# Performance work log

Hardware: AMD Instinct MI355X
Metric: run time of the kernel (lower is better)

The kernel has to match this reference:

```python
import jax, jax.numpy as jnp
import numpy as np

TEMPERATURE = 0.1
EPS = 1e-12  # matches F.normalize eps clamp


def setup_inputs() -> dict:
    key = jax.random.key(0)
    k1, k2 = jax.random.split(key)
    B, D = 4096, 1024
    z1 = jax.random.normal(k1, (B, D), dtype=jnp.float32)
    z2 = jax.random.normal(k2, (B, D), dtype=jnp.float32)
    return {"z1": z1, "z2": z2}


def reference(z1, z2):
    B = z1.shape[0]
    # L2-normalize rows (F.normalize dim=1, eps clamp)
    n1 = z1 / jnp.maximum(jnp.linalg.norm(z1, axis=1, keepdims=True), EPS)
    n2 = z2 / jnp.maximum(jnp.linalg.norm(z2, axis=1, keepdims=True), EPS)
    reps = jnp.concatenate([n1, n2], axis=0)  # [2B, D]
    # Rows are unit-norm, so cosine similarity == dot product -> one GEMM
    sim = (reps @ reps.T) / TEMPERATURE  # [2B, 2B]
    # positives: diag offsets +B and -B
    pos = jnp.concatenate([jnp.diagonal(sim, B), jnp.diagonal(sim, -B)])  # [2B]
    # logits row i = [pos_i, sim[i, j != i]]. logsumexp over that set =
    # logaddexp(pos_i, logsumexp over the row with the main diagonal removed).
    eye = jnp.eye(2 * B, dtype=bool)
    masked = jnp.where(eye, -jnp.inf, sim)
    lse_neg = jax.scipy.special.logsumexp(masked, axis=1)  # [2B]
    lse = jnp.logaddexp(pos, lse_neg)
    # CrossEntropyLoss with labels==0 -> mean(lse - logit_0) = mean(lse - pos)
    return jnp.mean(lse - pos)
```

## Files before the change

### kernel.cpp

```cpp
#include <hip/hip_runtime.h>

#define D_DIM 1024
#define B_HALF 4096
#define NROWS 8192
#define INV_TEMP 10.0f

typedef __bf16 bf16x8 __attribute__((ext_vector_type(8)));
typedef float floatx4 __attribute__((ext_vector_type(4)));

__device__ __forceinline__ unsigned short f32_to_bf16(float f) {
    union { float f; unsigned u; } v; v.f = f;
    unsigned r = 0x7FFFu + ((v.u >> 16) & 1u);
    return (unsigned short)((v.u + r) >> 16);
}

__global__ __launch_bounds__(256) void normalize_kernel(
    const float* __restrict__ z1, const float* __restrict__ z2,
    unsigned short* __restrict__ R)
{
    const int row = blockIdx.x;
    const int tid = threadIdx.x;
    const float* src = (row < B_HALF) ? (z1 + (size_t)row * D_DIM)
                                      : (z2 + (size_t)(row - B_HALF) * D_DIM);
    float4 v = ((const float4*)src)[tid];
    float ss = v.x * v.x + v.y * v.y + v.z * v.z + v.w * v.w;
    #pragma unroll
    for (int off = 32; off > 0; off >>= 1) ss += __shfl_down(ss, off);
    __shared__ float wsum[4];
    if ((tid & 63) == 0) wsum[tid >> 6] = ss;
    __syncthreads();
    float tot = wsum[0] + wsum[1] + wsum[2] + wsum[3];
    float scale = 1.0f / fmaxf(sqrtf(tot), 1e-12f);
    ushort4 o;
    o.x = f32_to_bf16(v.x * scale);
    o.y = f32_to_bf16(v.y * scale);
    o.z = f32_to_bf16(v.z * scale);
    o.w = f32_to_bf16(v.w * scale);
    ((ushort4*)(R + (size_t)row * D_DIM))[tid] = o;
}

__global__ __launch_bounds__(256) void gemm_lse_kernel(
    const unsigned short* __restrict__ R,
    float* __restrict__ partial, float* __restrict__ pos)
{
    __shared__ unsigned short As[128 * 32];
    __shared__ unsigned short Bs[128 * 32];
    __shared__ float rowsum[2][128];
    __shared__ float colsum[2][128];

    const int t = blockIdx.x;
    int rt = (int)((129.0f - sqrtf((float)(16641 - 8 * t))) * 0.5f);
    while ((rt + 1) * 64 - (rt + 1) * rt / 2 <= t) ++rt;
    while (rt * 64 - rt * (rt - 1) / 2 > t) --rt;
    const int ct = rt + (t - (rt * 64 - rt * (rt - 1) / 2));
    const bool isDiag = (rt == ct);

    const int tid = threadIdx.x;
    const int wave = tid >> 6, lane = tid & 63;
    const int wm = wave >> 1, wn = wave & 1;
    const int row0 = rt * 128, col0 = ct * 128;

    floatx4 acc[4][4] = {};

    const int lrow = lane >> 2;
    const int lk = (lane & 3) * 8;
    const unsigned short* gA = R + (size_t)row0 * D_DIM;
    const unsigned short* gB = R + (size_t)col0 * D_DIM;

    const int lm = lane & 15;
    const int lq = lane >> 4;

    for (int k0 = 0; k0 < D_DIM; k0 += 32) {
        #pragma unroll
        for (int rnd = 0; rnd < 2; ++rnd) {
            const int c = rnd * 4 + wave;
            const int grow = c * 16 + lrow;
            __builtin_amdgcn_global_load_lds(
                (const __attribute__((address_space(1))) unsigned int*)(gA + (size_t)grow * D_DIM + k0 + lk),
                (__attribute__((address_space(3))) unsigned int*)(As + c * 512),
                16, 0, 0);
            __builtin_amdgcn_global_load_lds(
                (const __attribute__((address_space(1))) unsigned int*)(gB + (size_t)grow * D_DIM + k0 + lk),
                (__attribute__((address_space(3))) unsigned int*)(Bs + c * 512),
                16, 0, 0);
        }
        __syncthreads();

        bf16x8 af[4], bfr[4];
        #pragma unroll
        for (int i = 0; i < 4; ++i) {
            af[i]  = *(const bf16x8*)(As + (wm * 64 + i * 16 + lm) * 32 + lq * 8);
            bfr[i] = *(const bf16x8*)(Bs + (wn * 64 + i * 16 + lm) * 32 + lq * 8);
        }
        #pragma unroll
        for (int mi = 0; mi < 4; ++mi)
            #pragma unroll
            for (int ni = 0; ni < 4; ++ni)
                acc[mi][ni] = __builtin_amdgcn_mfma_f32_16x16x32_bf16(
                    af[mi], bfr[ni], acc[mi][ni], 0, 0, 0);
        __syncthreads();
    }

    float ecol[4] = {0.0f, 0.0f, 0.0f, 0.0f};
    #pragma unroll
    for (int mi = 0; mi < 4; ++mi) {
        #pragma unroll
        for (int reg = 0; reg < 4; ++reg) {
            const int gr = row0 + wm * 64 + mi * 16 + lq * 4 + reg;
            float esum = 0.0f;
            #pragma unroll
            for (int ni = 0; ni < 4; ++ni) {
                const int gc = col0 + wn * 64 + ni * 16 + lm;
                float s = acc[mi][ni][reg] * INV_TEMP;
                if (gc == gr + B_HALF) { pos[gr] = s; pos[gc] = s; }
                float e = (gc == gr) ? 0.0f : __expf(s);
                esum += e;
                ecol[ni] += e;
            }
            esum += __shfl_xor(esum, 1);
            esum += __shfl_xor(esum, 2);
            esum += __shfl_xor(esum, 4);
            esum += __shfl_xor(esum, 8);
            if (lm == 0) rowsum[wn][wm * 64 + mi * 16 + lq * 4 + reg] = esum;
        }
    }
    #pragma unroll
    for (int ni = 0; ni < 4; ++ni) {
        ecol[ni] += __shfl_xor(ecol[ni], 16);
        ecol[ni] += __shfl_xor(ecol[ni], 32);
    }
    if (lq == 0 && !isDiag) {
        #pragma unroll
        for (int ni = 0; ni < 4; ++ni)
            colsum[wm][wn * 64 + ni * 16 + lm] = ecol[ni];
    }
    __syncthreads();
    if (tid < 128) {
        partial[(size_t)(row0 + tid) * 64 + ct] = rowsum[0][tid] + rowsum[1][tid];
        if (!isDiag)
            partial[(size_t)(col0 + tid) * 64 + rt] = colsum[0][tid] + colsum[1][tid];
    }
}

__global__ __launch_bounds__(256) void finalize_kernel(
    const float* __restrict__ partial, const float* __restrict__ pos,
    float* __restrict__ out)
{
    const int r = blockIdx.x * 256 + threadIdx.x;
    const float4* p = (const float4*)(partial + (size_t)r * 64);
    float S = 0.0f;
    #pragma unroll
    for (int i = 0; i < 16; ++i) { float4 v = p[i]; S += (v.x + v.y) + (v.z + v.w); }
    const float po = pos[r];
    float contrib = log1pf(S * __expf(-po));
    #pragma unroll
    for (int off = 32; off > 0; off >>= 1) contrib += __shfl_down(contrib, off);
    __shared__ float wsum[4];
    if ((threadIdx.x & 63) == 0) wsum[threadIdx.x >> 6] = contrib;
    __syncthreads();
    if (threadIdx.x == 0)
        atomicAdd(out, (wsum[0] + wsum[1] + wsum[2] + wsum[3]) * (1.0f / 8192.0f));
}

extern "C" void kernel_launch(void* const* d_in, const int* in_sizes, int n_in,
                              void* d_out, int out_size, void* d_ws, size_t ws_size,
                              hipStream_t stream)
{
    const float* z1 = (const float*)d_in[0];
    const float* z2 = (const float*)d_in[1];
    float* out = (float*)d_out;
    char* ws = (char*)d_ws;
    unsigned short* R = (unsigned short*)ws;
    float* partial = (float*)(ws + (size_t)16 * 1024 * 1024);
    float* pos     = (float*)(ws + (size_t)18 * 1024 * 1024);

    hipMemsetAsync(d_out, 0, sizeof(float), stream);
    normalize_kernel<<<NROWS, 256, 0, stream>>>(z1, z2, R);
    gemm_lse_kernel<<<2080, 256, 0, stream>>>(R, partial, pos);
    finalize_kernel<<<32, 256, 0, stream>>>(partial, pos, out);
}
```

Before: 174.7 us.

## Fuse normalize, GEMM-LSE and finalize into one persistent cooperative kernel

Replaces the three-kernel pipeline with a single cooperative persistent kernel. It normalizes rows, synchronizes the grid, hands out triangular GEMM tiles through an atomic work counter, synchronizes again, and finalizes the loss in block 0. Per-tile row and column exp-sums now go to a per-row float array via atomics, replacing the 64-wide partial buffer. This is meant to remove launch overhead, the memset and the partial-sum traffic. In exchange it adds grid-sync cost, atomic contention, a serial single-block finalize, and nondeterministic float summation order. A fallback three-kernel path runs only if the cooperative launch fails.

```diff
diff --git a/kernel.cpp b/kernel.cpp
--- a/kernel.cpp
+++ b/kernel.cpp
@@ -1,9 +1,13 @@
 #include <hip/hip_runtime.h>
+#include <hip/hip_cooperative_groups.h>
+
+namespace cg = cooperative_groups;
 
 #define D_DIM 1024
 #define B_HALF 4096
 #define NROWS 8192
 #define INV_TEMP 10.0f
+#define NTILES 2080
 
 typedef __bf16 bf16x8 __attribute__((ext_vector_type(8)));
 typedef float floatx4 __attribute__((ext_vector_type(4)));
@@ -14,61 +18,33 @@
     return (unsigned short)((v.u + r) >> 16);
 }
 
-__global__ __launch_bounds__(256) void normalize_kernel(
-    const float* __restrict__ z1, const float* __restrict__ z2,
-    unsigned short* __restrict__ R)
-{
-    const int row = blockIdx.x;
-    const int tid = threadIdx.x;
-    const float* src = (row < B_HALF) ? (z1 + (size_t)row * D_DIM)
-                                      : (z2 + (size_t)(row - B_HALF) * D_DIM);
-    float4 v = ((const float4*)src)[tid];
-    float ss = v.x * v.x + v.y * v.y + v.z * v.z + v.w * v.w;
-    #pragma unroll
-    for (int off = 32; off > 0; off >>= 1) ss += __shfl_down(ss, off);
-    __shared__ float wsum[4];
-    if ((tid & 63) == 0) wsum[tid >> 6] = ss;
-    __syncthreads();
-    float tot = wsum[0] + wsum[1] + wsum[2] + wsum[3];
-    float scale = 1.0f / fmaxf(sqrtf(tot), 1e-12f);
-    ushort4 o;
-    o.x = f32_to_bf16(v.x * scale);
-    o.y = f32_to_bf16(v.y * scale);
-    o.z = f32_to_bf16(v.z * scale);
-    o.w = f32_to_bf16(v.w * scale);
-    ((ushort4*)(R + (size_t)row * D_DIM))[tid] = o;
-}
-
-__global__ __launch_bounds__(256) void gemm_lse_kernel(
-    const unsigned short* __restrict__ R,
-    float* __restrict__ partial, float* __restrict__ pos)
+__device__ __forceinline__ void process_tile(
+    int t, const unsigned short* __restrict__ R,
+    float* __restrict__ Srow, float* __restrict__ pos, int tid)
 {
     __shared__ unsigned short As[128 * 32];
     __shared__ unsigned short Bs[128 * 32];
     __shared__ float rowsum[2][128];
     __shared__ float colsum[2][128];
 
-    const int t = blockIdx.x;
+    const int wave = tid >> 6, lane = tid & 63;
+    const int wm = wave >> 1, wn = wave & 1;
+    const int lrow = lane >> 2;
+    const int lk = (lane & 3) * 8;
+    const int lm = lane & 15;
+    const int lq = lane >> 4;
+
     int rt = (int)((129.0f - sqrtf((float)(16641 - 8 * t))) * 0.5f);
     while ((rt + 1) * 64 - (rt + 1) * rt / 2 <= t) ++rt;
     while (rt * 64 - rt * (rt - 1) / 2 > t) --rt;
     const int ct = rt + (t - (rt * 64 - rt * (rt - 1) / 2));
     const bool isDiag = (rt == ct);
-
-    const int tid = threadIdx.x;
-    const int wave = tid >> 6, lane = tid & 63;
-    const int wm = wave >> 1, wn = wave & 1;
     const int row0 = rt * 128, col0 = ct * 128;
 
-    floatx4 acc[4][4] = {};
-
-    const int lrow = lane >> 2;
-    const int lk = (lane & 3) * 8;
     const unsigned short* gA = R + (size_t)row0 * D_DIM;
     const unsigned short* gB = R + (size_t)col0 * D_DIM;
 
-    const int lm = lane & 15;
-    const int lq = lane >> 4;
+    floatx4 acc[4][4] = {};
 
     for (int k0 = 0; k0 < D_DIM; k0 += 32) {
         #pragma unroll
@@ -136,27 +112,117 @@
     }
     __syncthreads();
     if (tid < 128) {
-        partial[(size_t)(row0 + tid) * 64 + ct] = rowsum[0][tid] + rowsum[1][tid];
+        unsafeAtomicAdd(&Srow[row0 + tid], rowsum[0][tid] + rowsum[1][tid]);
         if (!isDiag)
-            partial[(size_t)(col0 + tid) * 64 + rt] = colsum[0][tid] + colsum[1][tid];
-    }
+            unsafeAtomicAdd(&Srow[col0 + tid], colsum[0][tid] + colsum[1][tid]);
+    }
+    __syncthreads();
+}
+
+__global__ __launch_bounds__(256) void fused_kernel(
+    const float* __restrict__ z1, const float* __restrict__ z2,
+    unsigned short* __restrict__ R, float* __restrict__ Srow,
+    float* __restrict__ pos, unsigned int* __restrict__ ctr,
+    float* __restrict__ out)
+{
+    __shared__ float red[4];
+    __shared__ int s_t;
+    const int tid = threadIdx.x;
+    const int bid = blockIdx.x;
+    const int nb = gridDim.x;
+    const int wave = tid >> 6, lane = tid & 63;
+
+    if (bid == 0 && tid == 0) ctr[0] = 0u;
+    for (int row = bid; row < NROWS; row += nb) {
+        const float* src = (row < B_HALF) ? (z1 + (size_t)row * D_DIM)
+                                          : (z2 + (size_t)(row - B_HALF) * D_DIM);
+        float4 v = ((const float4*)src)[tid];
+        float ss = v.x * v.x + v.y * v.y + v.z * v.z + v.w * v.w;
+        #pragma unroll
+        for (int off = 32; off > 0; off >>= 1) ss += __shfl_down(ss, off);
+        if (lane == 0) red[wave] = ss;
+        __syncthreads();
+        float tot = red[0] + red[1] + red[2] + red[3];
+        float scale = 1.0f / fmaxf(sqrtf(tot), 1e-12f);
+        ushort4 o;
+        o.x = f32_to_bf16(v.x * scale);
+        o.y = f32_to_bf16(v.y * scale);
+        o.z = f32_to_bf16(v.z * scale);
+        o.w = f32_to_bf16(v.w * scale);
+        ((ushort4*)(R + (size_t)row * D_DIM))[tid] = o;
+        if (tid == 0) Srow[row] = 0.0f;
+        __syncthreads();
+    }
+    cg::this_grid().sync();
+
+    for (;;) {
+        if (tid == 0) s_t = (int)atomicAdd(ctr, 1u);
+        __syncthreads();
+        const int t = s_t;
+        if (t >= NTILES) break;
+        process_tile(t, R, Srow, pos, tid);
+    }
+    cg::this_grid().sync();
+
+    if (bid == 0) {
+        float c = 0.0f;
+        for (int r = tid; r < NROWS; r += 256)
+            c += log1pf(Srow[r] * __expf(-pos[r]));
+        #pragma unroll
+        for (int off = 32; off > 0; off >>= 1) c += __shfl_down(c, off);
+        __syncthreads();
+        if (lane == 0) red[wave] = c;
+        __syncthreads();
+        if (tid == 0)
+            out[0] = (red[0] + red[1] + red[2] + red[3]) * (1.0f / 8192.0f);
+    }
+}
+
+__global__ __launch_bounds__(256) void normalize_kernel(
+    const float* __restrict__ z1, const float* __restrict__ z2,
+    unsigned short* __restrict__ R, float* __restrict__ Srow,
+    float* __restrict__ out)
+{
+    const int row = blockIdx.x;
+    const int tid = threadIdx.x;
+    if (row == 0 && tid == 0) out[0] = 0.0f;
+    const float* src = (row < B_HALF) ? (z1 + (size_t)row * D_DIM)
+                                      : (z2 + (size_t)(row - B_HALF) * D_DIM);
+    float4 v = ((const float4*)src)[tid];
+    float ss = v.x * v.x + v.y * v.y + v.z * v.z + v.w * v.w;
+    #pragma unroll
+    for (int off = 32; off > 0; off >>= 1) ss += __shfl_down(ss, off);
+    __shared__ float wsum[4];
+    if ((tid & 63) == 0) wsum[tid >> 6] = ss;
+    __syncthreads();
+    float tot = wsum[0] + wsum[1] + wsum[2] + wsum[3];
+    float scale = 1.0f / fmaxf(sqrtf(tot), 1e-12f);
+    ushort4 o;
+    o.x = f32_to_bf16(v.x * scale);
+    o.y = f32_to_bf16(v.y * scale);
+    o.z = f32_to_bf16(v.z * scale);
+    o.w = f32_to_bf16(v.w * scale);
+    ((ushort4*)(R + (size_t)row * D_DIM))[tid] = o;
+    if (tid == 0) Srow[row] = 0.0f;
+}
+
+__global__ __launch_bounds__(256) void gemm_kernel(
+    const unsigned short* __restrict__ R,
+    float* __restrict__ Srow, float* __restrict__ pos)
+{
+    process_tile(blockIdx.x, R, Srow, pos, threadIdx.x);
 }
 
 __global__ __launch_bounds__(256) void finalize_kernel(
-    const float* __restrict__ partial, const float* __restrict__ pos,
+    const float* __restrict__ Srow, const float* __restrict__ pos,
     float* __restrict__ out)
 {
     const int r = blockIdx.x * 256 + threadIdx.x;
-    const float4* p = (const float4*)(partial + (size_t)r * 64);
-    float S = 0.0f;
-    #pragma unroll
-    for (int i = 0; i < 16; ++i) { float4 v = p[i]; S += (v.x + v.y) + (v.z + v.w); }
-    const float po = pos[r];
-    float contrib = log1pf(S * __expf(-po));
-    #pragma unroll
-    for (int off = 32; off > 0; off >>= 1) contrib += __shfl_down(contrib, off);
+    float c = log1pf(Srow[r] * __expf(-pos[r]));
+    #pragma unroll
+    for (int off = 32; off > 0; off >>= 1) c += __shfl_down(c, off);
     __shared__ float wsum[4];
-    if ((threadIdx.x & 63) == 0) wsum[threadIdx.x >> 6] = contrib;
+    if ((threadIdx.x & 63) == 0) wsum[threadIdx.x >> 6] = c;
     __syncthreads();
     if (threadIdx.x == 0)
         atomicAdd(out, (wsum[0] + wsum[1] + wsum[2] + wsum[3]) * (1.0f / 8192.0f));
@@ -171,11 +237,26 @@
     float* out = (float*)d_out;
     char* ws = (char*)d_ws;
     unsigned short* R = (unsigned short*)ws;
-    float* partial = (float*)(ws + (size_t)16 * 1024 * 1024);
-    float* pos     = (float*)(ws + (size_t)18 * 1024 * 1024);
-
-    hipMemsetAsync(d_out, 0, sizeof(float), stream);
-    normalize_kernel<<<NROWS, 256, 0, stream>>>(z1, z2, R);
-    gemm_lse_kernel<<<2080, 256, 0, stream>>>(R, partial, pos);
-    finalize_kernel<<<32, 256, 0, stream>>>(partial, pos, out);
-}
+    float* Srow = (float*)(ws + (size_t)16 * 1024 * 1024);
+    float* pos  = (float*)(ws + (size_t)16 * 1024 * 1024 + 32768);
+    unsigned int* ctr = (unsigned int*)(ws + (size_t)16 * 1024 * 1024 + 65536);
+
+    int nPerCU = 0;
+    hipError_t oe = hipOccupancyMaxActiveBlocksPerMultiprocessor(
+        &nPerCU, fused_kernel, 256, 0);
+    int grid = (oe == hipSuccess && nPerCU > 0) ? nPerCU * 256 : 0;
+    if (grid > NTILES) grid = NTILES;
+
+    hipError_t e = hipErrorUnknown;
+    if (grid >= 256) {
+        void* args[] = { (void*)&z1, (void*)&z2, (void*)&R, (void*)&Srow,
+                         (void*)&pos, (void*)&ctr, (void*)&out };
+        e = hipLaunchCooperativeKernel((const void*)fused_kernel,
+                                       dim3(grid), dim3(256), args, 0, stream);
+    }
+    if (e != hipSuccess) {
+        normalize_kernel<<<NROWS, 256, 0, stream>>>(z1, z2, R, Srow, out);
+        gemm_kernel<<<NTILES, 256, 0, stream>>>(R, Srow, pos);
+        finalize_kernel<<<32, 256, 0, stream>>>(Srow, pos, out);
+    }
+}
```

New measurement: 359.7 us. 2.06x slower.

## Switch similarity GEMM to FP8 scaled MFMA with atomic row-sum accumulation

Applied to the files above, without the earlier changes.

Normalized rows are now quantized to FP8 instead of bf16, and the GEMM uses the 16x16x128 scaled f8f6f4 MFMA with a K-step of 128 and a new LDS layout. This halves operand bytes and cuts the number of MFMA issues and barriers. Per-tile row and column exp-sums are atomically added into a per-row array instead of a 64-wide partial matrix, so finalize becomes a single read per row. The output memset is folded into the normalize kernel. FP8 precision loses accuracy in the logits, which are scaled by 10 before exp, so tolerance is at risk.

```diff
diff --git a/kernel.cpp b/kernel.cpp
--- a/kernel.cpp
+++ b/kernel.cpp
@@ -4,22 +4,20 @@
 #define B_HALF 4096
 #define NROWS 8192
 #define INV_TEMP 10.0f
+#define NTILES 2080
 
-typedef __bf16 bf16x8 __attribute__((ext_vector_type(8)));
 typedef float floatx4 __attribute__((ext_vector_type(4)));
-
-__device__ __forceinline__ unsigned short f32_to_bf16(float f) {
-    union { float f; unsigned u; } v; v.f = f;
-    unsigned r = 0x7FFFu + ((v.u >> 16) & 1u);
-    return (unsigned short)((v.u + r) >> 16);
-}
+typedef int i32x4 __attribute__((ext_vector_type(4)));
+typedef int i32x8 __attribute__((ext_vector_type(8)));
 
 __global__ __launch_bounds__(256) void normalize_kernel(
     const float* __restrict__ z1, const float* __restrict__ z2,
-    unsigned short* __restrict__ R)
+    unsigned char* __restrict__ R, float* __restrict__ Srow,
+    float* __restrict__ out)
 {
     const int row = blockIdx.x;
     const int tid = threadIdx.x;
+    if (row == 0 && tid == 0) out[0] = 0.0f;
     const float* src = (row < B_HALF) ? (z1 + (size_t)row * D_DIM)
                                       : (z2 + (size_t)(row - B_HALF) * D_DIM);
     float4 v = ((const float4*)src)[tid];
@@ -31,20 +29,18 @@
     __syncthreads();
     float tot = wsum[0] + wsum[1] + wsum[2] + wsum[3];
     float scale = 1.0f / fmaxf(sqrtf(tot), 1e-12f);
-    ushort4 o;
-    o.x = f32_to_bf16(v.x * scale);
-    o.y = f32_to_bf16(v.y * scale);
-    o.z = f32_to_bf16(v.z * scale);
-    o.w = f32_to_bf16(v.w * scale);
-    ((ushort4*)(R + (size_t)row * D_DIM))[tid] = o;
+    int w = __builtin_amdgcn_cvt_pk_fp8_f32(v.x * scale, v.y * scale, 0, false);
+    w = __builtin_amdgcn_cvt_pk_fp8_f32(v.z * scale, v.w * scale, w, true);
+    ((int*)(R + (size_t)row * D_DIM))[tid] = w;
+    if (tid == 0) Srow[row] = 0.0f;
 }
 
-__global__ __launch_bounds__(256) void gemm_lse_kernel(
-    const unsigned short* __restrict__ R,
-    float* __restrict__ partial, float* __restrict__ pos)
+__global__ __launch_bounds__(256) void gemm_kernel(
+    const unsigned char* __restrict__ R,
+    float* __restrict__ Srow, float* __restrict__ pos)
 {
-    __shared__ unsigned short As[128 * 32];
-    __shared__ unsigned short Bs[128 * 32];
+    __shared__ __align__(16) unsigned char As[16384];
+    __shared__ __align__(16) unsigned char Bs[16384];
     __shared__ float rowsum[2][128];
     __shared__ float colsum[2][128];
 
@@ -54,50 +50,60 @@
     while (rt * 64 - rt * (rt - 1) / 2 > t) --rt;
     const int ct = rt + (t - (rt * 64 - rt * (rt - 1) / 2));
     const bool isDiag = (rt == ct);
+    const int row0 = rt * 128, col0 = ct * 128;
 
     const int tid = threadIdx.x;
     const int wave = tid >> 6, lane = tid & 63;
     const int wm = wave >> 1, wn = wave & 1;
-    const int row0 = rt * 128, col0 = ct * 128;
+    const int lm = lane & 15;
+    const int lq = lane >> 4;
+
+    const unsigned char* gA = R + (size_t)row0 * D_DIM;
+    const unsigned char* gB = R + (size_t)col0 * D_DIM;
+
+    const int srow = lane & 15;
+    const int kgrp = (lane >> 4) * 32;
 
     floatx4 acc[4][4] = {};
 
-    const int lrow = lane >> 2;
-    const int lk = (lane & 3) * 8;
-    const unsigned short* gA = R + (size_t)row0 * D_DIM;
-    const unsigned short* gB = R + (size_t)col0 * D_DIM;
-
-    const int lm = lane & 15;
-    const int lq = lane >> 4;
-
-    for (int k0 = 0; k0 < D_DIM; k0 += 32) {
+    for (int k0 = 0; k0 < D_DIM; k0 += 128) {
         #pragma unroll
-        for (int rnd = 0; rnd < 2; ++rnd) {
-            const int c = rnd * 4 + wave;
-            const int grow = c * 16 + lrow;
+        for (int h = 0; h < 8; ++h) {
+            const int c = h * 4 + wave;
+            const int cc = c & 15;
+            const int mc = cc >> 1, g = cc & 1;
+            const unsigned char* gsrc = ((c < 16) ? gA : gB)
+                + (size_t)(mc * 16 + srow) * D_DIM + k0 + kgrp + g * 16;
+            unsigned char* ldst = ((c < 16) ? As : Bs) + (cc << 10);
             __builtin_amdgcn_global_load_lds(
-                (const __attribute__((address_space(1))) unsigned int*)(gA + (size_t)grow * D_DIM + k0 + lk),
-                (__attribute__((address_space(3))) unsigned int*)(As + c * 512),
-                16, 0, 0);
-            __builtin_amdgcn_global_load_lds(
-                (const __attribute__((address_space(1))) unsigned int*)(gB + (size_t)grow * D_DIM + k0 + lk),
-                (__attribute__((address_space(3))) unsigned int*)(Bs + c * 512),
+                (const __attribute__((address_space(1))) unsigned int*)gsrc,
+                (__attribute__((address_space(3))) unsigned int*)ldst,
                 16, 0, 0);
         }
         __syncthreads();
 
-        bf16x8 af[4], bfr[4];
+        i32x8 af[4], bfr[4];
         #pragma unroll
         for (int i = 0; i < 4; ++i) {
-            af[i]  = *(const bf16x8*)(As + (wm * 64 + i * 16 + lm) * 32 + lq * 8);
-            bfr[i] = *(const bf16x8*)(Bs + (wn * 64 + i * 16 + lm) * 32 + lq * 8);
+            union { i32x8 v8; struct { i32x4 lo, hi; } p; } ua, ub;
+            const int ca = (wm * 4 + i) * 2;
+            ua.p.lo = *(const i32x4*)(As + (ca << 10) + lane * 16);
+            ua.p.hi = *(const i32x4*)(As + ((ca + 1) << 10) + lane * 16);
+            af[i] = ua.v8;
+            const int cb = (wn * 4 + i) * 2;
+            ub.p.lo = *(const i32x4*)(Bs + (cb << 10) + lane * 16);
+            ub.p.hi = *(const i32x4*)(Bs + ((cb + 1) << 10) + lane * 16);
+            bfr[i] = ub.v8;
         }
         #pragma unroll
         for (int mi = 0; mi < 4; ++mi)
             #pragma unroll
             for (int ni = 0; ni < 4; ++ni)
-                acc[mi][ni] = __builtin_amdgcn_mfma_f32_16x16x32_bf16(
-                    af[mi], bfr[ni], acc[mi][ni], 0, 0, 0);
+                acc[mi][ni] = __builtin_amdgcn_mfma_scale_f32_16x16x128_f8f6f4(
+                    af[mi], bfr[ni], acc[mi][ni],
+                    0, 0,
+                    0, 0x7F7F7F7F,
+                    0, 0x7F7F7F7F);
         __syncthreads();
     }
 
@@ -136,27 +142,22 @@
     }
     __syncthreads();
     if (tid < 128) {
-        partial[(size_t)(row0 + tid) * 64 + ct] = rowsum[0][tid] + rowsum[1][tid];
+        unsafeAtomicAdd(&Srow[row0 + tid], rowsum[0][tid] + rowsum[1][tid]);
         if (!isDiag)
-            partial[(size_t)(col0 + tid) * 64 + rt] = colsum[0][tid] + colsum[1][tid];
+            unsafeAtomicAdd(&Srow[col0 + tid], colsum[0][tid] + colsum[1][tid]);
     }
 }
 
 __global__ __launch_bounds__(256) void finalize_kernel(
-    const float* __restrict__ partial, const float* __restrict__ pos,
+    const float* __restrict__ Srow, const float* __restrict__ pos,
     float* __restrict__ out)
 {
     const int r = blockIdx.x * 256 + threadIdx.x;
-    const float4* p = (const float4*)(partial + (size_t)r * 64);
-    float S = 0.0f;
+    float c = log1pf(Srow[r] * __expf(-pos[r]));
     #pragma unroll
-    for (int i = 0; i < 16; ++i) { float4 v = p[i]; S += (v.x + v.y) + (v.z + v.w); }
-    const float po = pos[r];
-    float contrib = log1pf(S * __expf(-po));
-    #pragma unroll
-    for (int off = 32; off > 0; off >>= 1) contrib += __shfl_down(contrib, off);
+    for (int off = 32; off > 0; off >>= 1) c += __shfl_down(c, off);
     __shared__ float wsum[4];
-    if ((threadIdx.x & 63) == 0) wsum[threadIdx.x >> 6] = contrib;
+    if ((threadIdx.x & 63) == 0) wsum[threadIdx.x >> 6] = c;
     __syncthreads();
     if (threadIdx.x == 0)
         atomicAdd(out, (wsum[0] + wsum[1] + wsum[2] + wsum[3]) * (1.0f / 8192.0f));
@@ -170,12 +171,11 @@
     const float* z2 = (const float*)d_in[1];
     float* out = (float*)d_out;
     char* ws = (char*)d_ws;
-    unsigned short* R = (unsigned short*)ws;
-    float* partial = (float*)(ws + (size_t)16 * 1024 * 1024);
-    float* pos     = (float*)(ws + (size_t)18 * 1024 * 1024);
+    unsigned char* R = (unsigned char*)ws;
+    float* Srow = (float*)(ws + (size_t)8 * 1024 * 1024);
+    float* pos  = (float*)(ws + (size_t)8 * 1024 * 1024 + 32768);
 
-    hipMemsetAsync(d_out, 0, sizeof(float), stream);
-    normalize_kernel<<<NROWS, 256, 0, stream>>>(z1, z2, R);
-    gemm_lse_kernel<<<2080, 256, 0, stream>>>(R, partial, pos);
-    finalize_kernel<<<32, 256, 0, stream>>>(partial, pos, out);
+    normalize_kernel<<<NROWS, 256, 0, stream>>>(z1, z2, R, Srow, out);
+    gemm_kernel<<<NTILES, 256, 0, stream>>>(R, Srow, pos);
+    finalize_kernel<<<32, 256, 0, stream>>>(Srow, pos, out);
 }
```

Result: slower. 215.2 us (+23.2%).
